# Kernel optimization log

Measured on AMD Instinct MI355X. Metric: run time of the kernel, lower is better.

The kernel has to match this reference:

```python
import jax, jax.numpy as jnp
import numpy as np

SIGMA = 1.0

def setup_inputs() -> dict:
    key = jax.random.key(0)
    k1, k2 = jax.random.split(key)
    N, IN, OUT = 524288, 64, 128
    x = jax.random.normal(k1, (N, IN), dtype=jnp.float32)
    bin_centers = jax.random.normal(k2, (OUT, IN), dtype=jnp.float32)
    return {"x": x, "bin_centers": bin_centers}

def reference(x, bin_centers):
    # distances[n,o] = sum_i (x[n,i] - c[o,i])^2 = ||x_n||^2 - 2 x_n.c_o + ||c_o||^2
    x2 = jnp.sum(x * x, axis=1)[:, None]                # [N,1]
    c2 = jnp.sum(bin_centers * bin_centers, axis=1)[None, :]  # [1,O]
    xc = jnp.einsum('ni,oi->no', x, bin_centers)        # [N,O] GEMM
    distances = x2 - 2.0 * xc + c2                      # [N,O]
    rbf = jnp.exp(-distances / (2.0 * SIGMA ** 2))      # [N,O]
    # histogram[o,i] = sum_n rbf[n,o] * x[n,i]  ->  rbf^T @ x
    histogram = jnp.einsum('no,ni->oi', rbf, x)         # [O,I] GEMM
    return histogram
```

## Files before the change

### kernel.cpp

```cpp
#include <hip/hip_runtime.h>
#include <stdint.h>


typedef __bf16 bf16x8 __attribute__((ext_vector_type(8)));
typedef unsigned short ushortx8 __attribute__((ext_vector_type(8)));
typedef unsigned short ushortx4 __attribute__((ext_vector_type(4)));
typedef float floatx4 __attribute__((ext_vector_type(4)));

#define LOG2E 1.4426950408889634f
#define GRIDN 768
#define NTILES 8192

#if __has_builtin(__builtin_amdgcn_exp2f)
#define EXP2F(x) __builtin_amdgcn_exp2f(x)
#else
#define EXP2F(x) exp2f(x)
#endif

static __device__ __forceinline__ unsigned short f2bf(float f) {
  unsigned int u = __float_as_uint(f);
  u += 0x7fffu + ((u >> 16) & 1u);
  return (unsigned short)(u >> 16);
}
static __device__ __forceinline__ float bf2f(unsigned short h) {
  return __uint_as_float(((unsigned int)h) << 16);
}

static __device__ __forceinline__ floatx4 mfma_bf16(ushortx8 a, ushortx8 b, floatx4 c) {
  return __builtin_amdgcn_mfma_f32_16x16x32_bf16(
      __builtin_bit_cast(bf16x8, a), __builtin_bit_cast(bf16x8, b), c, 0, 0, 0);
}

#define LSTR 72

__global__ __launch_bounds__(256, 3) void rbf_hist_kernel(
    const float* __restrict__ x, const float* __restrict__ c,
    float* __restrict__ out, float* __restrict__ ws, int use_ws) {
  __shared__ unsigned short sXhi[64][LSTR];
  __shared__ unsigned short sXlo[64][LSTR];
  __shared__ unsigned short sXT [64][LSTR];
  __shared__ unsigned short sP  [128][LSTR];
  __shared__ float          sX2 [64];

  const int t    = threadIdx.x;
  const int lane = t & 63;
  const int w    = t >> 6;
  const int l15  = lane & 15;
  const int quad = lane >> 4;

  ushortx8 chi[2][2], clo[2][2];
  float c2r[2];
#pragma unroll
  for (int oo = 0; oo < 2; ++oo) {
    const int ot = 2 * w + oo;
    float sq = 0.f;
#pragma unroll
    for (int s = 0; s < 2; ++s) {
      const float* p = c + (ot * 16 + l15) * 64 + s * 32 + quad * 8;
      float4 va = *(const float4*)(p);
      float4 vb = *(const float4*)(p + 4);
      float f[8] = {va.x, va.y, va.z, va.w, vb.x, vb.y, vb.z, vb.w};
      ushortx8 hv, lv;
#pragma unroll
      for (int j = 0; j < 8; ++j) {
        sq += f[j] * f[j];
        unsigned short hh = f2bf(f[j]);
        hv[j] = hh;
        lv[j] = f2bf(f[j] - bf2f(hh));
      }
      chi[oo][s] = hv;
      clo[oo][s] = lv;
    }
    sq += __shfl_xor(sq, 16);
    sq += __shfl_xor(sq, 32);
    c2r[oo] = sq;
  }

  floatx4 hacc[2][4];
#pragma unroll
  for (int a = 0; a < 2; ++a)
#pragma unroll
    for (int b = 0; b < 4; ++b) {
      floatx4 z = {0.f, 0.f, 0.f, 0.f};
      hacc[a][b] = z;
    }

  const int r = t >> 2, q = t & 3;
  float4 v[4];
  {
    const size_t row0 = (size_t)(blockIdx.x * 64 + r) * 64;
#pragma unroll
    for (int g = 0; g < 4; ++g)
      v[g] = *(const float4*)(x + row0 + q * 4 + g * 16);
  }

  for (int tile = blockIdx.x; tile < NTILES; tile += GRIDN) {
    __syncthreads();

    {
      float sq = 0.f;
#pragma unroll
      for (int g = 0; g < 4; ++g) {
        const int col = q * 4 + g * 16;
        float f[4] = {v[g].x, v[g].y, v[g].z, v[g].w};
        ushortx4 hv, lv;
#pragma unroll
        for (int j = 0; j < 4; ++j) {
          sq += f[j] * f[j];
          unsigned short hh = f2bf(f[j]);
          hv[j] = hh;
          lv[j] = f2bf(f[j] - bf2f(hh));
          sXT[col + j][r] = hh;
        }
        *(ushortx4*)&sXhi[r][col] = hv;
        *(ushortx4*)&sXlo[r][col] = lv;
      }
      sq += __shfl_xor(sq, 1);
      sq += __shfl_xor(sq, 2);
      if (q == 0) sX2[r] = sq;
    }

    if (tile + GRIDN < NTILES) {
      const size_t nrow = (size_t)((tile + GRIDN) * 64 + r) * 64;
#pragma unroll
      for (int g = 0; g < 4; ++g)
        v[g] = *(const float4*)(x + nrow + q * 4 + g * 16);
    }
    __syncthreads();

#pragma unroll
    for (int nt = 0; nt < 4; ++nt) {
      ushortx8 xh0 = *(const ushortx8*)&sXhi[nt * 16 + l15][quad * 8];
      ushortx8 xh1 = *(const ushortx8*)&sXhi[nt * 16 + l15][32 + quad * 8];
      ushortx8 xl0 = *(const ushortx8*)&sXlo[nt * 16 + l15][quad * 8];
      ushortx8 xl1 = *(const ushortx8*)&sXlo[nt * 16 + l15][32 + quad * 8];
      float x2v[4];
#pragma unroll
      for (int e = 0; e < 4; ++e) x2v[e] = sX2[nt * 16 + quad * 4 + e];

#pragma unroll
      for (int oo = 0; oo < 2; ++oo) {
        floatx4 acc;
#pragma unroll
        for (int e = 0; e < 4; ++e) acc[e] = -0.5f * (x2v[e] + c2r[oo]);
        acc = mfma_bf16(xh0, chi[oo][0], acc);
        acc = mfma_bf16(xh1, chi[oo][1], acc);
        acc = mfma_bf16(xh0, clo[oo][0], acc);
        acc = mfma_bf16(xh1, clo[oo][1], acc);
        acc = mfma_bf16(xl0, chi[oo][0], acc);
        acc = mfma_bf16(xl1, chi[oo][1], acc);
        unsigned short rb[4];
#pragma unroll
        for (int e = 0; e < 4; ++e) rb[e] = f2bf(EXP2F(acc[e] * LOG2E));
        const int o = (2 * w + oo) * 16 + l15;
        const int n0 = nt * 16 + quad * 4;
        *(unsigned int*)&sP[o][n0]     = (unsigned int)rb[0] | ((unsigned int)rb[1] << 16);
        *(unsigned int*)&sP[o][n0 + 2] = (unsigned int)rb[2] | ((unsigned int)rb[3] << 16);
      }
    }
    __syncthreads();

#pragma unroll
    for (int s = 0; s < 2; ++s) {
      ushortx8 a0 = *(const ushortx8*)&sP[(2 * w)     * 16 + l15][s * 32 + quad * 8];
      ushortx8 a1 = *(const ushortx8*)&sP[(2 * w + 1) * 16 + l15][s * 32 + quad * 8];
#pragma unroll
      for (int itl = 0; itl < 4; ++itl) {
        ushortx8 b = *(const ushortx8*)&sXT[itl * 16 + l15][s * 32 + quad * 8];
        hacc[0][itl] = mfma_bf16(a0, b, hacc[0][itl]);
        hacc[1][itl] = mfma_bf16(a1, b, hacc[1][itl]);
      }
    }
  }

  if (use_ws) {
    float* part = ws + (size_t)blockIdx.x * 8192;
#pragma unroll
    for (int oi = 0; oi < 2; ++oi)
#pragma unroll
      for (int itl = 0; itl < 4; ++itl)
#pragma unroll
        for (int e = 0; e < 4; ++e) {
          int o = (2 * w + oi) * 16 + quad * 4 + e;
          int i = itl * 16 + l15;
          part[o * 64 + i] = hacc[oi][itl][e];
        }
  } else {
#pragma unroll
    for (int oi = 0; oi < 2; ++oi)
#pragma unroll
      for (int itl = 0; itl < 4; ++itl)
#pragma unroll
        for (int e = 0; e < 4; ++e) {
          int o = (2 * w + oi) * 16 + quad * 4 + e;
          int i = itl * 16 + l15;
          atomicAdd(out + o * 64 + i, hacc[oi][itl][e]);
        }
  }
}

__global__ void reduce_kernel(const float* __restrict__ ws, float* __restrict__ out) {
  const int tid = blockIdx.x * 256 + threadIdx.x;
  const int e = tid & 8191;
  const int half = tid >> 13;
  const float* p = ws + (size_t)half * 384 * 8192 + e;
  float s = 0.f;
#pragma unroll 8
  for (int b = 0; b < 384; ++b) s += p[(size_t)b * 8192];
  atomicAdd(out + e, s);
}

__global__ void zero_out_kernel(float* out, int n) {
  int i = blockIdx.x * 256 + threadIdx.x;
  if (i < n) out[i] = 0.f;
}

extern "C" void kernel_launch(void* const* d_in, const int* in_sizes, int n_in,
                              void* d_out, int out_size, void* d_ws, size_t ws_size,
                              hipStream_t stream) {
  (void)in_sizes; (void)n_in;
  const float* x = (const float*)d_in[0];
  const float* c = (const float*)d_in[1];
  float* out = (float*)d_out;
  float* ws  = (float*)d_ws;

  const int use_ws = (ws_size >= (size_t)GRIDN * 8192 * sizeof(float)) ? 1 : 0;

  zero_out_kernel<<<(out_size + 255) / 256, 256, 0, stream>>>(out, out_size);
  rbf_hist_kernel<<<GRIDN, 256, 0, stream>>>(x, c, out, ws, use_ws);
  if (use_ws)
    reduce_kernel<<<64, 256, 0, stream>>>(ws, out);
}
```

Measured before the change: 213.6 us.

## Use per-wave P buffers, fold log2e scaling into inputs, raise grid to 1024

Replaces the block-wide shared rbf buffer and its extra barrier with a small per-wave buffer. Each wave now computes exp for two n-subtiles and then immediately feeds the histogram MFMAs. Pre-scales x and the centers by sqrt(log2e) so the exponent becomes a single exp2 with no multiply, and packs bf16 conversions in pairs. Grid grows to 1024 blocks with occupancy 4 and a fixed iteration count, and the reduction kernel is adjusted to match. This trades a larger workspace and more register pressure for fewer syncs and less LDS traffic.

```diff
diff --git a/kernel.cpp b/kernel.cpp
--- a/kernel.cpp
+++ b/kernel.cpp
@@ -4,12 +4,11 @@
 
 typedef __bf16 bf16x8 __attribute__((ext_vector_type(8)));
 typedef unsigned short ushortx8 __attribute__((ext_vector_type(8)));
-typedef unsigned short ushortx4 __attribute__((ext_vector_type(4)));
 typedef float floatx4 __attribute__((ext_vector_type(4)));
 
-#define LOG2E 1.4426950408889634f
-#define GRIDN 768
-#define NTILES 8192
+#define GRIDN 1024
+#define NITER 8
+#define SCL 1.2011224087864498f
 
 #if __has_builtin(__builtin_amdgcn_exp2f)
 #define EXP2F(x) __builtin_amdgcn_exp2f(x)
@@ -17,13 +16,12 @@
 #define EXP2F(x) exp2f(x)
 #endif
 
-static __device__ __forceinline__ unsigned short f2bf(float f) {
+static __device__ __forceinline__ unsigned int bfbits(float f) {
   unsigned int u = __float_as_uint(f);
-  u += 0x7fffu + ((u >> 16) & 1u);
-  return (unsigned short)(u >> 16);
-}
-static __device__ __forceinline__ float bf2f(unsigned short h) {
-  return __uint_as_float(((unsigned int)h) << 16);
+  return u + 0x7fffu + ((u >> 16) & 1u);
+}
+static __device__ __forceinline__ unsigned int pkbf(float a, float b) {
+  return (bfbits(a) >> 16) | (bfbits(b) & 0xffff0000u);
 }
 
 static __device__ __forceinline__ floatx4 mfma_bf16(ushortx8 a, ushortx8 b, floatx4 c) {
@@ -32,14 +30,15 @@
 }
 
 #define LSTR 72
-
-__global__ __launch_bounds__(256, 3) void rbf_hist_kernel(
+#define PSTR 40
+
+__global__ __launch_bounds__(256, 4) void rbf_hist_kernel(
     const float* __restrict__ x, const float* __restrict__ c,
     float* __restrict__ out, float* __restrict__ ws, int use_ws) {
   __shared__ unsigned short sXhi[64][LSTR];
   __shared__ unsigned short sXlo[64][LSTR];
   __shared__ unsigned short sXT [64][LSTR];
-  __shared__ unsigned short sP  [128][LSTR];
+  __shared__ unsigned short sPw [4][32][PSTR];
   __shared__ float          sX2 [64];
 
   const int t    = threadIdx.x;
@@ -48,8 +47,8 @@
   const int l15  = lane & 15;
   const int quad = lane >> 4;
 
-  ushortx8 chi[2][2], clo[2][2];
-  float c2r[2];
+  uint4 chi[2][2], clo[2][2];
+  float m2c[2];
 #pragma unroll
   for (int oo = 0; oo < 2; ++oo) {
     const int ot = 2 * w + oo;
@@ -60,20 +59,24 @@
       float4 va = *(const float4*)(p);
       float4 vb = *(const float4*)(p + 4);
       float f[8] = {va.x, va.y, va.z, va.w, vb.x, vb.y, vb.z, vb.w};
-      ushortx8 hv, lv;
-#pragma unroll
-      for (int j = 0; j < 8; ++j) {
-        sq += f[j] * f[j];
-        unsigned short hh = f2bf(f[j]);
-        hv[j] = hh;
-        lv[j] = f2bf(f[j] - bf2f(hh));
-      }
-      chi[oo][s] = hv;
-      clo[oo][s] = lv;
+      unsigned int h[4], l[4];
+#pragma unroll
+      for (int jp = 0; jp < 4; ++jp) {
+        float a = f[2 * jp] * SCL, b = f[2 * jp + 1] * SCL;
+        sq = fmaf(a, a, sq);
+        sq = fmaf(b, b, sq);
+        unsigned int hp = pkbf(a, b);
+        float la = a - __uint_as_float(hp << 16);
+        float lb = b - __uint_as_float(hp & 0xffff0000u);
+        h[jp] = hp;
+        l[jp] = pkbf(la, lb);
+      }
+      chi[oo][s] = uint4{h[0], h[1], h[2], h[3]};
+      clo[oo][s] = uint4{l[0], l[1], l[2], l[3]};
     }
     sq += __shfl_xor(sq, 16);
     sq += __shfl_xor(sq, 32);
-    c2r[oo] = sq;
+    m2c[oo] = -0.5f * sq;
   }
 
   floatx4 hacc[2][4];
@@ -94,7 +97,7 @@
       v[g] = *(const float4*)(x + row0 + q * 4 + g * 16);
   }
 
-  for (int tile = blockIdx.x; tile < NTILES; tile += GRIDN) {
+  for (int it = 0; it < NITER; ++it) {
     __syncthreads();
 
     {
@@ -102,26 +105,32 @@
 #pragma unroll
       for (int g = 0; g < 4; ++g) {
         const int col = q * 4 + g * 16;
-        float f[4] = {v[g].x, v[g].y, v[g].z, v[g].w};
-        ushortx4 hv, lv;
-#pragma unroll
-        for (int j = 0; j < 4; ++j) {
-          sq += f[j] * f[j];
-          unsigned short hh = f2bf(f[j]);
-          hv[j] = hh;
-          lv[j] = f2bf(f[j] - bf2f(hh));
-          sXT[col + j][r] = hh;
-        }
-        *(ushortx4*)&sXhi[r][col] = hv;
-        *(ushortx4*)&sXlo[r][col] = lv;
+        float f0 = v[g].x, f1 = v[g].y, f2 = v[g].z, f3 = v[g].w;
+        unsigned int u01 = pkbf(f0, f1), u23 = pkbf(f2, f3);
+        sXT[col + 0][r] = (unsigned short)(u01 & 0xffffu);
+        sXT[col + 1][r] = (unsigned short)(u01 >> 16);
+        sXT[col + 2][r] = (unsigned short)(u23 & 0xffffu);
+        sXT[col + 3][r] = (unsigned short)(u23 >> 16);
+        float s0 = f0 * SCL, s1 = f1 * SCL, s2 = f2 * SCL, s3 = f3 * SCL;
+        sq = fmaf(s0, s0, sq); sq = fmaf(s1, s1, sq);
+        sq = fmaf(s2, s2, sq); sq = fmaf(s3, s3, sq);
+        unsigned int h01 = pkbf(s0, s1), h23 = pkbf(s2, s3);
+        float l0 = s0 - __uint_as_float(h01 << 16);
+        float l1 = s1 - __uint_as_float(h01 & 0xffff0000u);
+        float l2 = s2 - __uint_as_float(h23 << 16);
+        float l3 = s3 - __uint_as_float(h23 & 0xffff0000u);
+        uint2 hh = {h01, h23};
+        uint2 ll = {pkbf(l0, l1), pkbf(l2, l3)};
+        *(uint2*)&sXhi[r][col] = hh;
+        *(uint2*)&sXlo[r][col] = ll;
       }
       sq += __shfl_xor(sq, 1);
       sq += __shfl_xor(sq, 2);
-      if (q == 0) sX2[r] = sq;
-    }
-
-    if (tile + GRIDN < NTILES) {
-      const size_t nrow = (size_t)((tile + GRIDN) * 64 + r) * 64;
+      if (q == 0) sX2[r] = -0.5f * sq;
+    }
+
+    if (it < NITER - 1) {
+      const size_t nrow = (size_t)((blockIdx.x + (it + 1) * GRIDN) * 64 + r) * 64;
 #pragma unroll
       for (int g = 0; g < 4; ++g)
         v[g] = *(const float4*)(x + nrow + q * 4 + g * 16);
@@ -129,44 +138,38 @@
     __syncthreads();
 
 #pragma unroll
-    for (int nt = 0; nt < 4; ++nt) {
-      ushortx8 xh0 = *(const ushortx8*)&sXhi[nt * 16 + l15][quad * 8];
-      ushortx8 xh1 = *(const ushortx8*)&sXhi[nt * 16 + l15][32 + quad * 8];
-      ushortx8 xl0 = *(const ushortx8*)&sXlo[nt * 16 + l15][quad * 8];
-      ushortx8 xl1 = *(const ushortx8*)&sXlo[nt * 16 + l15][32 + quad * 8];
-      float x2v[4];
-#pragma unroll
-      for (int e = 0; e < 4; ++e) x2v[e] = sX2[nt * 16 + quad * 4 + e];
-
-#pragma unroll
-      for (int oo = 0; oo < 2; ++oo) {
-        floatx4 acc;
-#pragma unroll
-        for (int e = 0; e < 4; ++e) acc[e] = -0.5f * (x2v[e] + c2r[oo]);
-        acc = mfma_bf16(xh0, chi[oo][0], acc);
-        acc = mfma_bf16(xh1, chi[oo][1], acc);
-        acc = mfma_bf16(xh0, clo[oo][0], acc);
-        acc = mfma_bf16(xh1, clo[oo][1], acc);
-        acc = mfma_bf16(xl0, chi[oo][0], acc);
-        acc = mfma_bf16(xl1, chi[oo][1], acc);
-        unsigned short rb[4];
-#pragma unroll
-        for (int e = 0; e < 4; ++e) rb[e] = f2bf(EXP2F(acc[e] * LOG2E));
-        const int o = (2 * w + oo) * 16 + l15;
-        const int n0 = nt * 16 + quad * 4;
-        *(unsigned int*)&sP[o][n0]     = (unsigned int)rb[0] | ((unsigned int)rb[1] << 16);
-        *(unsigned int*)&sP[o][n0 + 2] = (unsigned int)rb[2] | ((unsigned int)rb[3] << 16);
-      }
-    }
-    __syncthreads();
-
-#pragma unroll
-    for (int s = 0; s < 2; ++s) {
-      ushortx8 a0 = *(const ushortx8*)&sP[(2 * w)     * 16 + l15][s * 32 + quad * 8];
-      ushortx8 a1 = *(const ushortx8*)&sP[(2 * w + 1) * 16 + l15][s * 32 + quad * 8];
+    for (int p = 0; p < 2; ++p) {
+#pragma unroll
+      for (int u = 0; u < 2; ++u) {
+        const int nt = 2 * p + u;
+        ushortx8 xh0 = *(const ushortx8*)&sXhi[nt * 16 + l15][quad * 8];
+        ushortx8 xh1 = *(const ushortx8*)&sXhi[nt * 16 + l15][32 + quad * 8];
+        ushortx8 xl0 = *(const ushortx8*)&sXlo[nt * 16 + l15][quad * 8];
+        ushortx8 xl1 = *(const ushortx8*)&sXlo[nt * 16 + l15][32 + quad * 8];
+        float4 m2x = *(const float4*)&sX2[nt * 16 + quad * 4];
+
+#pragma unroll
+        for (int oo = 0; oo < 2; ++oo) {
+          floatx4 acc = {m2x.x + m2c[oo], m2x.y + m2c[oo],
+                         m2x.z + m2c[oo], m2x.w + m2c[oo]};
+          acc = mfma_bf16(xh0, __builtin_bit_cast(ushortx8, chi[oo][0]), acc);
+          acc = mfma_bf16(xh1, __builtin_bit_cast(ushortx8, chi[oo][1]), acc);
+          acc = mfma_bf16(xh0, __builtin_bit_cast(ushortx8, clo[oo][0]), acc);
+          acc = mfma_bf16(xh1, __builtin_bit_cast(ushortx8, clo[oo][1]), acc);
+          acc = mfma_bf16(xl0, __builtin_bit_cast(ushortx8, chi[oo][0]), acc);
+          acc = mfma_bf16(xl1, __builtin_bit_cast(ushortx8, chi[oo][1]), acc);
+          unsigned int r01 = pkbf(EXP2F(acc[0]), EXP2F(acc[1]));
+          unsigned int r23 = pkbf(EXP2F(acc[2]), EXP2F(acc[3]));
+          unsigned short* bp = &sPw[w][oo * 16 + l15][u * 16 + quad * 4];
+          *(unsigned int*)(bp)     = r01;
+          *(unsigned int*)(bp + 2) = r23;
+        }
+      }
+      ushortx8 a0 = *(const ushortx8*)&sPw[w][l15][quad * 8];
+      ushortx8 a1 = *(const ushortx8*)&sPw[w][16 + l15][quad * 8];
 #pragma unroll
       for (int itl = 0; itl < 4; ++itl) {
-        ushortx8 b = *(const ushortx8*)&sXT[itl * 16 + l15][s * 32 + quad * 8];
+        ushortx8 b = *(const ushortx8*)&sXT[itl * 16 + l15][p * 32 + quad * 8];
         hacc[0][itl] = mfma_bf16(a0, b, hacc[0][itl]);
         hacc[1][itl] = mfma_bf16(a1, b, hacc[1][itl]);
       }
@@ -202,11 +205,11 @@
 __global__ void reduce_kernel(const float* __restrict__ ws, float* __restrict__ out) {
   const int tid = blockIdx.x * 256 + threadIdx.x;
   const int e = tid & 8191;
-  const int half = tid >> 13;
-  const float* p = ws + (size_t)half * 384 * 8192 + e;
+  const int part = tid >> 13;
+  const float* p = ws + (size_t)part * 256 * 8192 + e;
   float s = 0.f;
 #pragma unroll 8
-  for (int b = 0; b < 384; ++b) s += p[(size_t)b * 8192];
+  for (int b = 0; b < 256; ++b) s += p[(size_t)b * 8192];
   atomicAdd(out + e, s);
 }
 
@@ -229,5 +232,5 @@
   zero_out_kernel<<<(out_size + 255) / 256, 256, 0, stream>>>(out, out_size);
   rbf_hist_kernel<<<GRIDN, 256, 0, stream>>>(x, c, out, ws, use_ws);
   if (use_ws)
-    reduce_kernel<<<64, 256, 0, stream>>>(ws, out);
-}
+    reduce_kernel<<<128, 256, 0, stream>>>(ws, out);
+}
```

Result: slower. 219.2 us (+2.6%).
